# Optimization experiments

Hardware: AMD Instinct MI355X
Metric: run time of the kernel (lower is better)

## Reference

```python
import jax, jax.numpy as jnp
import numpy as np
import math

D_MODEL = 1024
N_HEADS = 16
HEAD_DIM = D_MODEL // N_HEADS
EPS = 1e-5


def setup_inputs() -> dict:
    key = jax.random.key(0)
    ks = jax.random.split(key, 16)
    B, S = 2, 2048
    s = 1.0 / math.sqrt(D_MODEL)
    inp = {
        "q": jax.random.normal(ks[0], (B, S, D_MODEL), jnp.float32),
        "k": jax.random.normal(ks[1], (B, S, D_MODEL), jnp.float32),
        "v": jax.random.normal(ks[2], (B, S, D_MODEL), jnp.float32),
        "attn_mask": jax.random.randint(ks[3], (B, S, S), 0, 2, jnp.int32),
        "wq": jax.random.normal(ks[4], (D_MODEL, D_MODEL), jnp.float32) * s,
        "bq": jnp.zeros((D_MODEL,), jnp.float32),
        "wk": jax.random.normal(ks[5], (D_MODEL, D_MODEL), jnp.float32) * s,
        "bk": jnp.zeros((D_MODEL,), jnp.float32),
        "wv": jax.random.normal(ks[6], (D_MODEL, D_MODEL), jnp.float32) * s,
        "bv": jnp.zeros((D_MODEL,), jnp.float32),
        "wo": jax.random.normal(ks[7], (D_MODEL, D_MODEL), jnp.float32) * s,
        "bo": jnp.zeros((D_MODEL,), jnp.float32),
        "gamma": jnp.ones((D_MODEL,), jnp.float32),
        "beta": jnp.zeros((D_MODEL,), jnp.float32),
    }
    return inp


def _layernorm(x, gamma, beta):
    mu = jnp.mean(x, axis=-1, keepdims=True)
    var = jnp.mean(jnp.square(x - mu), axis=-1, keepdims=True)
    return (x - mu) * jax.lax.rsqrt(var + EPS) * gamma + beta


def reference(q, k, v, attn_mask, wq, bq, wk, bk, wv, bv, wo, bo, gamma, beta):
    B, S, D = q.shape
    residual = q
    # projections; torch Linear: x @ W^T + b. Split heads -> [B, H, S, dh]
    qh = (q @ wq.T + bq).reshape(B, S, N_HEADS, HEAD_DIM).transpose(0, 2, 1, 3)
    kh = (k @ wk.T + bk).reshape(B, -1, N_HEADS, HEAD_DIM).transpose(0, 2, 1, 3)
    vh = (v @ wv.T + bv).reshape(B, -1, N_HEADS, HEAD_DIM).transpose(0, 2, 1, 3)
    scale = math.sqrt(HEAD_DIM)
    scores = jnp.einsum("bhqd,bhkd->bhqk", qh, kh) / scale  # [B,H,S,S]
    NEG_INF = 1000000000.0
    scores = jnp.where(attn_mask[:, None, :, :] == 0, -NEG_INF, scores)
    attention = jax.nn.softmax(scores, axis=-1)
    context = jnp.einsum("bhqk,bhkd->bhqd", attention, vh)
    context = context.transpose(0, 2, 1, 3).reshape(B, S, D)
    output = context @ wo.T + bo
    output = _layernorm(residual + output, gamma, beta)
    return output, attention
```

## Files before the change

### kernel.cpp

```cpp
#include <hip/hip_runtime.h>
#include <hip/hip_bf16.h>

#define B_  2
#define S_  2048
#define D_  1024
#define H_  16
#define DH_ 64

typedef __attribute__((ext_vector_type(8))) short short8;
typedef __attribute__((ext_vector_type(4))) float floatx4;

static __device__ __forceinline__ ushort f2b(float x) {
  union { __hip_bfloat16 h; ushort u; } cv;
  cv.h = __float2bfloat16(x);
  return cv.u;
}
static __device__ __forceinline__ float b2f(ushort u) {
  union { unsigned int i; float f; } cv;
  cv.i = (unsigned int)u << 16;
  return cv.f;
}

static __device__ __forceinline__ void gload16(const ushort* g, ushort* l) {
  __builtin_amdgcn_global_load_lds(
      (const __attribute__((address_space(1))) unsigned int*)g,
      (__attribute__((address_space(3))) unsigned int*)l, 16, 0, 0);
}

__global__ __launch_bounds__(256) void cast_f2b_kernel(
    const float* __restrict__ x, __hip_bfloat16* __restrict__ y, int n)
{
  int i = (blockIdx.x * 256 + threadIdx.x) * 4;
  if (i >= n) return;
  float4 v = *(const float4*)(x + i);
  union { __hip_bfloat16 h[4]; uint2 u; } cv;
  cv.h[0] = __float2bfloat16(v.x);
  cv.h[1] = __float2bfloat16(v.y);
  cv.h[2] = __float2bfloat16(v.z);
  cv.h[3] = __float2bfloat16(v.w);
  *(uint2*)((ushort*)y + i) = cv.u;
}

template<bool OUT_BF16>
__global__ __launch_bounds__(256) void mfma_gemm_kernel(
    const ushort* __restrict__ A, const ushort* __restrict__ Wt,
    const float* __restrict__ bias, void* __restrict__ Cout,
    int M, int N, int K)
{
  __shared__ ushort As[2][128 * 64];
  __shared__ ushort Bs[2][64 * 64];
  const int tid = threadIdx.x;
  const int l = tid & 63, w = tid >> 6;
  const int wm = w >> 1, wn = w & 1;
  const int lr = l & 15, lq = l >> 4;
  const int m0 = blockIdx.x * 128, n0 = blockIdx.y * 64;

  const int srow = l >> 3;
  const int scol = (l & 7) ^ srow;
  const ushort* Ag = A + (size_t)(m0 + w * 32 + srow) * K + scol * 8;
  const ushort* Bg = Wt + (size_t)(n0 + w * 16 + srow) * K + scol * 8;

  floatx4 acc[4][2];
#pragma unroll
  for (int tm = 0; tm < 4; ++tm)
#pragma unroll
    for (int tn = 0; tn < 2; ++tn) acc[tm][tn] = (floatx4)0.0f;

#pragma unroll
  for (int c = 0; c < 4; ++c)
    gload16(Ag + (size_t)(c * 8) * K, &As[0][(w * 32 + c * 8) * 64]);
#pragma unroll
  for (int c = 0; c < 2; ++c)
    gload16(Bg + (size_t)(c * 8) * K, &Bs[0][(w * 16 + c * 8) * 64]);
  __syncthreads();

  int cur = 0;
  for (int kt = 0; kt < K; kt += 64) {
    if (kt + 64 < K) {
      const int nb = cur ^ 1;
#pragma unroll
      for (int c = 0; c < 4; ++c)
        gload16(Ag + (size_t)(c * 8) * K + kt + 64, &As[nb][(w * 32 + c * 8) * 64]);
#pragma unroll
      for (int c = 0; c < 2; ++c)
        gload16(Bg + (size_t)(c * 8) * K + kt + 64, &Bs[nb][(w * 16 + c * 8) * 64]);
    }
#pragma unroll
    for (int s = 0; s < 2; ++s) {
      const int cx = ((s * 4 + lq) ^ (lr & 7)) * 8;
      short8 b[2];
#pragma unroll
      for (int tn = 0; tn < 2; ++tn)
        b[tn] = *(const short8*)&Bs[cur][(wn * 32 + tn * 16 + lr) * 64 + cx];
#pragma unroll
      for (int tm = 0; tm < 4; ++tm) {
        short8 a = *(const short8*)&As[cur][(wm * 64 + tm * 16 + lr) * 64 + cx];
#pragma unroll
        for (int tn = 0; tn < 2; ++tn)
          acc[tm][tn] = __builtin_amdgcn_mfma_f32_16x16x32_bf16(a, b[tn], acc[tm][tn], 0, 0, 0);
      }
    }
    __syncthreads();
    cur ^= 1;
  }

#pragma unroll
  for (int tm = 0; tm < 4; ++tm)
#pragma unroll
    for (int tn = 0; tn < 2; ++tn) {
      const int n = n0 + wn * 32 + tn * 16 + lr;
      const float bv = bias[n];
#pragma unroll
      for (int r = 0; r < 4; ++r) {
        const int m = m0 + wm * 64 + tm * 16 + lq * 4 + r;
        const float val = acc[tm][tn][r] + bv;
        if (OUT_BF16)
          ((__hip_bfloat16*)Cout)[(size_t)m * N + n] = __float2bfloat16(val);
        else
          ((float*)Cout)[(size_t)m * N + n] = val;
      }
    }
}

__global__ __launch_bounds__(256) void transpose_v_kernel(
    const ushort* __restrict__ Vh, ushort* __restrict__ Vt)
{
  __shared__ ushort T[64 * 72];
  const int tid = threadIdx.x;
  const int s0 = blockIdx.x * 64;
  const int h = blockIdx.y;
  const int b = blockIdx.z;
  const ushort* src = Vh + ((size_t)b * S_ + s0) * D_ + h * DH_;
#pragma unroll
  for (int i = 0; i < 2; ++i) {
    int f = tid + i * 256;
    int r = f >> 3, c = f & 7;
    *(uint4*)&T[r * 72 + c * 8] = *(const uint4*)(src + (size_t)r * D_ + c * 8);
  }
  __syncthreads();
  ushort* dst = Vt + (size_t)(b * H_ + h) * DH_ * S_ + s0;
#pragma unroll
  for (int i = 0; i < 2; ++i) {
    int f = tid + i * 256;
    int d = f >> 3, sc = f & 7;
    ushort tmp[8];
#pragma unroll
    for (int u = 0; u < 8; ++u) tmp[u] = T[(sc * 8 + u) * 72 + d];
    *(uint4*)(dst + (size_t)d * S_ + sc * 8) = *(uint4*)tmp;
  }
}

__global__ __launch_bounds__(256) void pack_mask_kernel(
    const int* __restrict__ mask, unsigned long long* __restrict__ bits)
{
  const int row = blockIdx.x;
  const int tid = threadIdx.x;
  const int* mr = mask + (size_t)row * S_;
  unsigned long long* br = bits + (size_t)row * (S_ / 64);
#pragma unroll
  for (int it = 0; it < S_ / 256; ++it) {
    const int j = it * 256 + tid;
    const unsigned long long bal = __ballot(mr[j] != 0);
    if ((tid & 63) == 0) br[it * 4 + (tid >> 6)] = bal;
  }
}

static __device__ __forceinline__ void qk_tile_swz(
    const short8 qf[2][2], const ushort* Kb, int lq, int lr, floatx4 acc[2][8])
{
#pragma unroll
  for (int s = 0; s < 2; ++s) {
    const int cx = ((s * 4 + lq) ^ (lr & 7)) * 8;
#pragma unroll
    for (int g = 0; g < 2; ++g) {
      short8 bb[4];
#pragma unroll
      for (int t = 0; t < 4; ++t)
        bb[t] = *(const short8*)&Kb[((g * 4 + t) * 16 + lr) * 64 + cx];
#pragma unroll
      for (int tm = 0; tm < 2; ++tm)
#pragma unroll
        for (int t = 0; t < 4; ++t)
          acc[tm][g * 4 + t] =
              __builtin_amdgcn_mfma_f32_16x16x32_bf16(qf[tm][s], bb[t], acc[tm][g * 4 + t], 0, 0, 0);
    }
  }
}

__global__ __launch_bounds__(256, 2) void flash_kernel(
    const ushort* __restrict__ Qh, const ushort* __restrict__ Kh,
    const ushort* __restrict__ Vt, const unsigned long long* __restrict__ mbits,
    float* __restrict__ attn, __hip_bfloat16* __restrict__ Ctx)
{
  __shared__ ushort Ks[128 * 64];
  __shared__ ushort Vs[64 * 128];
  __shared__ ushort Ps[128 * 136];

  const int tid = threadIdx.x;
  const int l = tid & 63, w = tid >> 6;
  const int lr = l & 15, lq = l >> 4;

  const int flat = blockIdx.x;
  const int swz = (flat & 7) * 64 + (flat >> 3);
  const int bh = swz >> 4, iblk = swz & 15;
  const int b = bh >> 4, h = bh & 15;
  const int i0 = iblk * 128;

  const unsigned long long* mb = mbits + (size_t)b * S_ * (S_ / 64);
  float* ab = attn + (size_t)bh * S_ * S_;
  const ushort* Vb = Vt + (size_t)bh * DH_ * S_;

  const int srow = l >> 3;
  const int scol = (l & 7) ^ srow;
  const ushort* Kg = Kh + ((size_t)b * S_ + w * 32 + srow) * D_ + h * DH_ + scol * 8;

  short8 qf[2][2];
#pragma unroll
  for (int tm = 0; tm < 2; ++tm)
#pragma unroll
    for (int s = 0; s < 2; ++s)
      qf[tm][s] = *(const short8*)&Qh[((size_t)b * S_ + i0 + w * 32 + tm * 16 + lr) * D_ +
                                      h * DH_ + s * 32 + lq * 8];

  float s_run[2][4];
#pragma unroll
  for (int tm = 0; tm < 2; ++tm)
#pragma unroll
    for (int r = 0; r < 4; ++r) s_run[tm][r] = 0.0f;

#pragma unroll
  for (int c = 0; c < 4; ++c)
    gload16(Kg + (size_t)(c * 8) * D_, &Ks[(w * 32 + c * 8) * 64]);
  __syncthreads();

  ushort* kcur = Ks;
  ushort* knxt = Vs;
  for (int jt = 0; jt < 16; ++jt) {
    if (jt < 15) {
#pragma unroll
      for (int c = 0; c < 4; ++c)
        gload16(Kg + (size_t)((jt + 1) * 128 + c * 8) * D_, &knxt[(w * 32 + c * 8) * 64]);
    }
    floatx4 acc[2][8];
#pragma unroll
    for (int tm = 0; tm < 2; ++tm)
#pragma unroll
      for (int tn = 0; tn < 8; ++tn) acc[tm][tn] = (floatx4)0.0f;
    qk_tile_swz(qf, kcur, lq, lr, acc);

#pragma unroll
    for (int tm = 0; tm < 2; ++tm)
#pragma unroll
      for (int r = 0; r < 4; ++r) {
        const int gi = i0 + w * 32 + tm * 16 + lq * 4 + r;
        const ulonglong2 mp = *(const ulonglong2*)&mb[(size_t)gi * 32 + jt * 2];
        float ts = 0.0f;
#pragma unroll
        for (int tn = 0; tn < 8; ++tn) {
          const unsigned long long mw = (tn < 4) ? mp.x : mp.y;
          const float s = acc[tm][tn][r] * 0.125f;
          ts += ((mw >> ((tn & 3) * 16 + lr)) & 1) ? __expf(s) : 0.0f;
        }
#pragma unroll
        for (int off = 1; off < 16; off <<= 1) ts += __shfl_xor(ts, off);
        s_run[tm][r] += ts;
      }
    __syncthreads();
    ushort* tp = kcur; kcur = knxt; knxt = tp;
  }

  float inv[2][4];
#pragma unroll
  for (int tm = 0; tm < 2; ++tm)
#pragma unroll
    for (int r = 0; r < 4; ++r) inv[tm][r] = 1.0f / s_run[tm][r];

  floatx4 acco[2][4];
#pragma unroll
  for (int tm = 0; tm < 2; ++tm)
#pragma unroll
    for (int t = 0; t < 4; ++t) acco[tm][t] = (floatx4)0.0f;

#pragma unroll
  for (int c = 0; c < 4; ++c)
    gload16(Kg + (size_t)(c * 8) * D_, &Ks[(w * 32 + c * 8) * 64]);

  const int vrow = l >> 4;
  const int vcol = l & 15;

  for (int jt = 0; jt < 16; ++jt) {
#pragma unroll
    for (int c = 0; c < 4; ++c) {
      const int r = w * 16 + c * 4 + vrow;
      const int c16 = vcol ^ ((r & 7) << 1);
      gload16(Vb + (size_t)r * S_ + jt * 128 + c16 * 8, &Vs[(w * 16 + c * 4) * 128]);
    }
    __syncthreads();

    floatx4 acc[2][8];
#pragma unroll
    for (int tm = 0; tm < 2; ++tm)
#pragma unroll
      for (int tn = 0; tn < 8; ++tn) acc[tm][tn] = (floatx4)0.0f;
    qk_tile_swz(qf, Ks, lq, lr, acc);

#pragma unroll
    for (int tm = 0; tm < 2; ++tm)
#pragma unroll
      for (int r = 0; r < 4; ++r) {
        const int gi = i0 + w * 32 + tm * 16 + lq * 4 + r;
        const ulonglong2 mp = *(const ulonglong2*)&mb[(size_t)gi * 32 + jt * 2];
        const float iv = inv[tm][r];
#pragma unroll
        for (int tn = 0; tn < 8; ++tn) {
          const unsigned long long mw = (tn < 4) ? mp.x : mp.y;
          const float s = acc[tm][tn][r] * 0.125f;
          acc[tm][tn][r] = ((mw >> ((tn & 3) * 16 + lr)) & 1) ? __expf(s) * iv : 0.0f;
        }
      }

#pragma unroll
    for (int tm = 0; tm < 2; ++tm)
#pragma unroll
      for (int tn = 0; tn < 8; ++tn)
#pragma unroll
        for (int r = 0; r < 4; ++r)
          Ps[(w * 32 + tm * 16 + lq * 4 + r) * 136 + tn * 16 + lr] = f2b(acc[tm][tn][r]);
    __syncthreads();

    if (jt < 15) {
#pragma unroll
      for (int c = 0; c < 4; ++c)
        gload16(Kg + (size_t)((jt + 1) * 128 + c * 8) * D_, &Ks[(w * 32 + c * 8) * 64]);
    }

#pragma unroll
    for (int it = 0; it < 8; ++it) {
      const int f = tid + it * 256;
      const int ri = f >> 4, cc = f & 15;
      const uint4 pv = *(const uint4*)&Ps[ri * 136 + cc * 8];
      const ushort* us = (const ushort*)&pv;
      float4 lo, hi;
      lo.x = b2f(us[0]); lo.y = b2f(us[1]); lo.z = b2f(us[2]); lo.w = b2f(us[3]);
      hi.x = b2f(us[4]); hi.y = b2f(us[5]); hi.z = b2f(us[6]); hi.w = b2f(us[7]);
      float4* dst = (float4*)(ab + (size_t)(i0 + ri) * S_ + jt * 128 + cc * 8);
      dst[0] = lo;
      dst[1] = hi;
    }

#pragma unroll
    for (int ch = 0; ch < 2; ++ch)
#pragma unroll
      for (int ks = 0; ks < 2; ++ks) {
        const int ko = ch * 64 + ks * 32 + lq * 8;
        const int c16 = (ch * 8 + ks * 4 + lq) ^ ((lr & 7) << 1);
        short8 bv[4];
#pragma unroll
        for (int t = 0; t < 4; ++t)
          bv[t] = *(const short8*)&Vs[(t * 16 + lr) * 128 + c16 * 8];
#pragma unroll
        for (int tm = 0; tm < 2; ++tm) {
          const short8 a = *(const short8*)&Ps[(w * 32 + tm * 16 + lr) * 136 + ko];
#pragma unroll
          for (int t = 0; t < 4; ++t)
            acco[tm][t] = __builtin_amdgcn_mfma_f32_16x16x32_bf16(a, bv[t], acco[tm][t], 0, 0, 0);
        }
      }
    __syncthreads();
  }

#pragma unroll
  for (int tm = 0; tm < 2; ++tm)
#pragma unroll
    for (int tn = 0; tn < 4; ++tn) {
      const int d = tn * 16 + lr;
#pragma unroll
      for (int r = 0; r < 4; ++r) {
        const int i = i0 + w * 32 + tm * 16 + lq * 4 + r;
        Ctx[((size_t)b * S_ + i) * D_ + h * DH_ + d] = __float2bfloat16(acco[tm][tn][r]);
      }
    }
}

__global__ __launch_bounds__(256) void ln_kernel(
    const float* __restrict__ resid, const float* __restrict__ Yo,
    const float* __restrict__ gamma, const float* __restrict__ beta,
    float* __restrict__ out)
{
  const size_t row = blockIdx.x;
  const float* r = resid + row * D_;
  const float* y = Yo + row * D_;
  const int tid = threadIdx.x;
  float x[4];
  float s = 0.0f;
#pragma unroll
  for (int i = 0; i < 4; ++i) {
    const int j = tid + i * 256;
    x[i] = r[j] + y[j];
    s += x[i];
  }
  __shared__ float red[4];
  const int lane = tid & 63, w = tid >> 6;
#pragma unroll
  for (int off = 32; off > 0; off >>= 1) s += __shfl_down(s, off);
  if (lane == 0) red[w] = s;
  __syncthreads();
  const float mu = (red[0] + red[1] + red[2] + red[3]) * (1.0f / D_);
  __syncthreads();

  float s2 = 0.0f;
#pragma unroll
  for (int i = 0; i < 4; ++i) {
    const float d = x[i] - mu;
    s2 += d * d;
  }
#pragma unroll
  for (int off = 32; off > 0; off >>= 1) s2 += __shfl_down(s2, off);
  if (lane == 0) red[w] = s2;
  __syncthreads();
  const float var = (red[0] + red[1] + red[2] + red[3]) * (1.0f / D_);
  const float rs = rsqrtf(var + 1e-5f);

#pragma unroll
  for (int i = 0; i < 4; ++i) {
    const int j = tid + i * 256;
    out[row * D_ + j] = (x[i] - mu) * rs * gamma[j] + beta[j];
  }
}

extern "C" void kernel_launch(void* const* d_in, const int* in_sizes, int n_in,
                              void* d_out, int out_size, void* d_ws, size_t ws_size,
                              hipStream_t stream) {
  (void)in_sizes; (void)n_in; (void)out_size; (void)ws_size;
  const float* q    = (const float*)d_in[0];
  const float* k    = (const float*)d_in[1];
  const float* v    = (const float*)d_in[2];
  const int*  mask  = (const int*)d_in[3];
  const float* wq   = (const float*)d_in[4];
  const float* bq   = (const float*)d_in[5];
  const float* wk   = (const float*)d_in[6];
  const float* bk   = (const float*)d_in[7];
  const float* wv   = (const float*)d_in[8];
  const float* bv   = (const float*)d_in[9];
  const float* wo   = (const float*)d_in[10];
  const float* bo   = (const float*)d_in[11];
  const float* gamma= (const float*)d_in[12];
  const float* beta = (const float*)d_in[13];

  const int M = B_ * S_;
  char* ws = (char*)d_ws;
  const size_t MBy = 1 << 20;
  ushort* qB  = (ushort*)(ws + 0);
  ushort* kB  = (ushort*)(ws + 8 * MBy);
  ushort* vB  = (ushort*)(ws + 16 * MBy);
  ushort* wqB = (ushort*)(ws + 24 * MBy);
  ushort* wkB = (ushort*)(ws + 26 * MBy);
  ushort* wvB = (ushort*)(ws + 28 * MBy);
  ushort* woB = (ushort*)(ws + 30 * MBy);
  ushort* Qh  = (ushort*)(ws + 32 * MBy);
  ushort* Kh  = (ushort*)(ws + 40 * MBy);
  ushort* Vh  = qB;
  ushort* Vt  = kB;
  __hip_bfloat16* Ctx = (__hip_bfloat16*)vB;
  float* Yo   = (float*)(ws + 32 * MBy);
  unsigned long long* mbits = (unsigned long long*)(ws + 0);

  float* out  = (float*)d_out;
  float* attn = out + (size_t)M * D_;

  cast_f2b_kernel<<<M * D_ / 1024, 256, 0, stream>>>(q, (__hip_bfloat16*)qB, M * D_);
  cast_f2b_kernel<<<M * D_ / 1024, 256, 0, stream>>>(k, (__hip_bfloat16*)kB, M * D_);
  cast_f2b_kernel<<<M * D_ / 1024, 256, 0, stream>>>(v, (__hip_bfloat16*)vB, M * D_);
  cast_f2b_kernel<<<D_ * D_ / 1024, 256, 0, stream>>>(wq, (__hip_bfloat16*)wqB, D_ * D_);
  cast_f2b_kernel<<<D_ * D_ / 1024, 256, 0, stream>>>(wk, (__hip_bfloat16*)wkB, D_ * D_);
  cast_f2b_kernel<<<D_ * D_ / 1024, 256, 0, stream>>>(wv, (__hip_bfloat16*)wvB, D_ * D_);
  cast_f2b_kernel<<<D_ * D_ / 1024, 256, 0, stream>>>(wo, (__hip_bfloat16*)woB, D_ * D_);

  dim3 pg(M / 128, D_ / 64);
  mfma_gemm_kernel<true><<<pg, 256, 0, stream>>>(qB, wqB, bq, Qh, M, D_, D_);
  mfma_gemm_kernel<true><<<pg, 256, 0, stream>>>(kB, wkB, bk, Kh, M, D_, D_);
  mfma_gemm_kernel<true><<<pg, 256, 0, stream>>>(vB, wvB, bv, Vh, M, D_, D_);

  transpose_v_kernel<<<dim3(S_ / 64, H_, B_), 256, 0, stream>>>(Vh, Vt);

  pack_mask_kernel<<<dim3(B_ * S_), 256, 0, stream>>>(mask, mbits);

  flash_kernel<<<dim3(B_ * H_ * S_ / 128), 256, 0, stream>>>(Qh, Kh, Vt, mbits, attn, Ctx);

  mfma_gemm_kernel<false><<<pg, 256, 0, stream>>>((const ushort*)Ctx, woB, bo, Yo, M, D_, D_);

  ln_kernel<<<dim3(M), 256, 0, stream>>>(q, Yo, gamma, beta, out);
}
```

Measured before the change: 851.4 us.

## Batch QKV GEMMs, double-buffer V tiles and swizzle P in flash kernel

The three projection GEMMs are merged into one launch over blockIdx.z, relying on the q/k/v and weight buffers sitting contiguously in the workspace. The V projection output is staged in the attention output buffer. In the flash kernel's second pass, V tiles are now double-buffered and prefetched alongside the next K tile, which removes one barrier per iteration. The padded P buffer is replaced by an XOR-swizzled 128-wide layout, saving LDS and aiming to avoid bank conflicts, at the cost of more LDS in use per block and reliance on the buffer-layout assumptions.

```diff
diff --git a/kernel.cpp b/kernel.cpp
--- a/kernel.cpp
+++ b/kernel.cpp
@@ -41,10 +41,11 @@
   *(uint2*)((ushort*)y + i) = cv.u;
 }
 
-template<bool OUT_BF16>
-__global__ __launch_bounds__(256) void mfma_gemm_kernel(
-    const ushort* __restrict__ A, const ushort* __restrict__ Wt,
-    const float* __restrict__ bias, void* __restrict__ Cout,
+__global__ __launch_bounds__(256, 3) void qkv_gemm_kernel(
+    const ushort* __restrict__ Aall, const ushort* __restrict__ Wall,
+    const float* __restrict__ b0, const float* __restrict__ b1,
+    const float* __restrict__ b2,
+    __hip_bfloat16* __restrict__ o01, __hip_bfloat16* __restrict__ o2,
     int M, int N, int K)
 {
   __shared__ ushort As[2][128 * 64];
@@ -54,6 +55,12 @@
   const int wm = w >> 1, wn = w & 1;
   const int lr = l & 15, lq = l >> 4;
   const int m0 = blockIdx.x * 128, n0 = blockIdx.y * 64;
+  const int z = blockIdx.z;
+
+  const ushort* A = Aall + (size_t)z * M * K;
+  const ushort* Wt = Wall + (size_t)z * N * K;
+  const float* bias = (z == 0) ? b0 : ((z == 1) ? b1 : b2);
+  __hip_bfloat16* Cout = (z == 2) ? o2 : (o01 + (size_t)z * M * N);
 
   const int srow = l >> 3;
   const int scol = (l & 7) ^ srow;
@@ -113,11 +120,83 @@
 #pragma unroll
       for (int r = 0; r < 4; ++r) {
         const int m = m0 + wm * 64 + tm * 16 + lq * 4 + r;
-        const float val = acc[tm][tn][r] + bv;
-        if (OUT_BF16)
-          ((__hip_bfloat16*)Cout)[(size_t)m * N + n] = __float2bfloat16(val);
-        else
-          ((float*)Cout)[(size_t)m * N + n] = val;
+        Cout[(size_t)m * N + n] = __float2bfloat16(acc[tm][tn][r] + bv);
+      }
+    }
+}
+
+__global__ __launch_bounds__(256, 3) void mfma_gemm_f32_kernel(
+    const ushort* __restrict__ A, const ushort* __restrict__ Wt,
+    const float* __restrict__ bias, float* __restrict__ Cout,
+    int M, int N, int K)
+{
+  __shared__ ushort As[2][128 * 64];
+  __shared__ ushort Bs[2][64 * 64];
+  const int tid = threadIdx.x;
+  const int l = tid & 63, w = tid >> 6;
+  const int wm = w >> 1, wn = w & 1;
+  const int lr = l & 15, lq = l >> 4;
+  const int m0 = blockIdx.x * 128, n0 = blockIdx.y * 64;
+
+  const int srow = l >> 3;
+  const int scol = (l & 7) ^ srow;
+  const ushort* Ag = A + (size_t)(m0 + w * 32 + srow) * K + scol * 8;
+  const ushort* Bg = Wt + (size_t)(n0 + w * 16 + srow) * K + scol * 8;
+
+  floatx4 acc[4][2];
+#pragma unroll
+  for (int tm = 0; tm < 4; ++tm)
+#pragma unroll
+    for (int tn = 0; tn < 2; ++tn) acc[tm][tn] = (floatx4)0.0f;
+
+#pragma unroll
+  for (int c = 0; c < 4; ++c)
+    gload16(Ag + (size_t)(c * 8) * K, &As[0][(w * 32 + c * 8) * 64]);
+#pragma unroll
+  for (int c = 0; c < 2; ++c)
+    gload16(Bg + (size_t)(c * 8) * K, &Bs[0][(w * 16 + c * 8) * 64]);
+  __syncthreads();
+
+  int cur = 0;
+  for (int kt = 0; kt < K; kt += 64) {
+    if (kt + 64 < K) {
+      const int nb = cur ^ 1;
+#pragma unroll
+      for (int c = 0; c < 4; ++c)
+        gload16(Ag + (size_t)(c * 8) * K + kt + 64, &As[nb][(w * 32 + c * 8) * 64]);
+#pragma unroll
+      for (int c = 0; c < 2; ++c)
+        gload16(Bg + (size_t)(c * 8) * K + kt + 64, &Bs[nb][(w * 16 + c * 8) * 64]);
+    }
+#pragma unroll
+    for (int s = 0; s < 2; ++s) {
+      const int cx = ((s * 4 + lq) ^ (lr & 7)) * 8;
+      short8 b[2];
+#pragma unroll
+      for (int tn = 0; tn < 2; ++tn)
+        b[tn] = *(const short8*)&Bs[cur][(wn * 32 + tn * 16 + lr) * 64 + cx];
+#pragma unroll
+      for (int tm = 0; tm < 4; ++tm) {
+        short8 a = *(const short8*)&As[cur][(wm * 64 + tm * 16 + lr) * 64 + cx];
+#pragma unroll
+        for (int tn = 0; tn < 2; ++tn)
+          acc[tm][tn] = __builtin_amdgcn_mfma_f32_16x16x32_bf16(a, b[tn], acc[tm][tn], 0, 0, 0);
+      }
+    }
+    __syncthreads();
+    cur ^= 1;
+  }
+
+#pragma unroll
+  for (int tm = 0; tm < 4; ++tm)
+#pragma unroll
+    for (int tn = 0; tn < 2; ++tn) {
+      const int n = n0 + wn * 32 + tn * 16 + lr;
+      const float bv = bias[n];
+#pragma unroll
+      for (int r = 0; r < 4; ++r) {
+        const int m = m0 + wm * 64 + tm * 16 + lq * 4 + r;
+        Cout[(size_t)m * N + n] = acc[tm][tn][r] + bv;
       }
     }
 }
@@ -193,8 +272,8 @@
     float* __restrict__ attn, __hip_bfloat16* __restrict__ Ctx)
 {
   __shared__ ushort Ks[128 * 64];
-  __shared__ ushort Vs[64 * 128];
-  __shared__ ushort Ps[128 * 136];
+  __shared__ ushort Vs[2][64 * 128];
+  __shared__ ushort Ps[128 * 128];
 
   const int tid = threadIdx.x;
   const int l = tid & 63, w = tid >> 6;
@@ -234,7 +313,7 @@
   __syncthreads();
 
   ushort* kcur = Ks;
-  ushort* knxt = Vs;
+  ushort* knxt = &Vs[0][0];
   for (int jt = 0; jt < 16; ++jt) {
     if (jt < 15) {
 #pragma unroll
@@ -281,20 +360,19 @@
 #pragma unroll
     for (int t = 0; t < 4; ++t) acco[tm][t] = (floatx4)0.0f;
 
+  const int vrow = l >> 4;
+  const int vcol = l & 15;
 #pragma unroll
   for (int c = 0; c < 4; ++c)
     gload16(Kg + (size_t)(c * 8) * D_, &Ks[(w * 32 + c * 8) * 64]);
-
-  const int vrow = l >> 4;
-  const int vcol = l & 15;
+#pragma unroll
+  for (int c = 0; c < 4; ++c) {
+    const int r = w * 16 + c * 4 + vrow;
+    const int c16 = vcol ^ ((r & 7) << 1);
+    gload16(Vb + (size_t)r * S_ + c16 * 8, &Vs[0][(w * 16 + c * 4) * 128]);
+  }
 
   for (int jt = 0; jt < 16; ++jt) {
-#pragma unroll
-    for (int c = 0; c < 4; ++c) {
-      const int r = w * 16 + c * 4 + vrow;
-      const int c16 = vcol ^ ((r & 7) << 1);
-      gload16(Vb + (size_t)r * S_ + jt * 128 + c16 * 8, &Vs[(w * 16 + c * 4) * 128]);
-    }
     __syncthreads();
 
     floatx4 acc[2][8];
@@ -324,21 +402,31 @@
 #pragma unroll
       for (int tn = 0; tn < 8; ++tn)
 #pragma unroll
-        for (int r = 0; r < 4; ++r)
-          Ps[(w * 32 + tm * 16 + lq * 4 + r) * 136 + tn * 16 + lr] = f2b(acc[tm][tn][r]);
+        for (int r = 0; r < 4; ++r) {
+          const int row = w * 32 + tm * 16 + lq * 4 + r;
+          const int unit = tn * 2 + (lr >> 3);
+          Ps[row * 128 + ((unit ^ (row & 15)) << 3) + (lr & 7)] = f2b(acc[tm][tn][r]);
+        }
     __syncthreads();
 
     if (jt < 15) {
 #pragma unroll
       for (int c = 0; c < 4; ++c)
         gload16(Kg + (size_t)((jt + 1) * 128 + c * 8) * D_, &Ks[(w * 32 + c * 8) * 64]);
+      ushort* vdst = &Vs[(jt + 1) & 1][0];
+#pragma unroll
+      for (int c = 0; c < 4; ++c) {
+        const int r = w * 16 + c * 4 + vrow;
+        const int c16 = vcol ^ ((r & 7) << 1);
+        gload16(Vb + (size_t)r * S_ + (jt + 1) * 128 + c16 * 8, &vdst[(w * 16 + c * 4) * 128]);
+      }
     }
 
 #pragma unroll
     for (int it = 0; it < 8; ++it) {
       const int f = tid + it * 256;
       const int ri = f >> 4, cc = f & 15;
-      const uint4 pv = *(const uint4*)&Ps[ri * 136 + cc * 8];
+      const uint4 pv = *(const uint4*)&Ps[ri * 128 + ((cc ^ (ri & 15)) << 3)];
       const ushort* us = (const ushort*)&pv;
       float4 lo, hi;
       lo.x = b2f(us[0]); lo.y = b2f(us[1]); lo.z = b2f(us[2]); lo.w = b2f(us[3]);
@@ -348,25 +436,26 @@
       dst[1] = hi;
     }
 
+    const ushort* vsrc = &Vs[jt & 1][0];
 #pragma unroll
     for (int ch = 0; ch < 2; ++ch)
 #pragma unroll
       for (int ks = 0; ks < 2; ++ks) {
-        const int ko = ch * 64 + ks * 32 + lq * 8;
-        const int c16 = (ch * 8 + ks * 4 + lq) ^ ((lr & 7) << 1);
+        const int u = ch * 8 + ks * 4 + lq;
+        const int c16 = u ^ ((lr & 7) << 1);
         short8 bv[4];
 #pragma unroll
         for (int t = 0; t < 4; ++t)
-          bv[t] = *(const short8*)&Vs[(t * 16 + lr) * 128 + c16 * 8];
+          bv[t] = *(const short8*)&vsrc[(t * 16 + lr) * 128 + c16 * 8];
 #pragma unroll
         for (int tm = 0; tm < 2; ++tm) {
-          const short8 a = *(const short8*)&Ps[(w * 32 + tm * 16 + lr) * 136 + ko];
+          const int row = w * 32 + tm * 16 + lr;
+          const short8 a = *(const short8*)&Ps[row * 128 + ((u ^ (row & 15)) << 3)];
 #pragma unroll
           for (int t = 0; t < 4; ++t)
             acco[tm][t] = __builtin_amdgcn_mfma_f32_16x16x32_bf16(a, bv[t], acco[tm][t], 0, 0, 0);
         }
       }
-    __syncthreads();
   }
 
 #pragma unroll
@@ -459,7 +548,6 @@
   ushort* woB = (ushort*)(ws + 30 * MBy);
   ushort* Qh  = (ushort*)(ws + 32 * MBy);
   ushort* Kh  = (ushort*)(ws + 40 * MBy);
-  ushort* Vh  = qB;
   ushort* Vt  = kB;
   __hip_bfloat16* Ctx = (__hip_bfloat16*)vB;
   float* Yo   = (float*)(ws + 32 * MBy);
@@ -467,6 +555,9 @@
 
   float* out  = (float*)d_out;
   float* attn = out + (size_t)M * D_;
+  ushort* Vh  = (ushort*)attn;
+
+  (void)wkB; (void)wvB;
 
   cast_f2b_kernel<<<M * D_ / 1024, 256, 0, stream>>>(q, (__hip_bfloat16*)qB, M * D_);
   cast_f2b_kernel<<<M * D_ / 1024, 256, 0, stream>>>(k, (__hip_bfloat16*)kB, M * D_);
@@ -476,10 +567,8 @@
   cast_f2b_kernel<<<D_ * D_ / 1024, 256, 0, stream>>>(wv, (__hip_bfloat16*)wvB, D_ * D_);
   cast_f2b_kernel<<<D_ * D_ / 1024, 256, 0, stream>>>(wo, (__hip_bfloat16*)woB, D_ * D_);
 
-  dim3 pg(M / 128, D_ / 64);
-  mfma_gemm_kernel<true><<<pg, 256, 0, stream>>>(qB, wqB, bq, Qh, M, D_, D_);
-  mfma_gemm_kernel<true><<<pg, 256, 0, stream>>>(kB, wkB, bk, Kh, M, D_, D_);
-  mfma_gemm_kernel<true><<<pg, 256, 0, stream>>>(vB, wvB, bv, Vh, M, D_, D_);
+  qkv_gemm_kernel<<<dim3(M / 128, D_ / 64, 3), 256, 0, stream>>>(
+      qB, wqB, bq, bk, bv, (__hip_bfloat16*)Qh, (__hip_bfloat16*)Vh, M, D_, D_);
 
   transpose_v_kernel<<<dim3(S_ / 64, H_, B_), 256, 0, stream>>>(Vh, Vt);
 
@@ -487,7 +576,8 @@
 
   flash_kernel<<<dim3(B_ * H_ * S_ / 128), 256, 0, stream>>>(Qh, Kh, Vt, mbits, attn, Ctx);
 
-  mfma_gemm_kernel<false><<<pg, 256, 0, stream>>>((const ushort*)Ctx, woB, bo, Yo, M, D_, D_);
+  mfma_gemm_f32_kernel<<<dim3(M / 128, D_ / 64), 256, 0, stream>>>(
+      (const ushort*)Ctx, woB, bo, Yo, M, D_, D_);
 
   ln_kernel<<<dim3(M), 256, 0, stream>>>(q, Yo, gamma, beta, out);
 }
```

Result: slower. 877.8 us (+3.1%).
